# Kernel optimization log

Measured on AMD Instinct MI355X. Metric: run time of the kernel, lower is better.

## Reference

```python
import jax, jax.numpy as jnp
import numpy as np

B, S, D, H = 2, 2048, 2048, 16
HD = D // H
EPS = 1e-5


def layernorm(x, scale, shift):
    mean = jnp.mean(x, axis=-1, keepdims=True)
    var = jnp.mean((x - mean) ** 2, axis=-1, keepdims=True)  # unbiased=False
    return scale * (x - mean) / jnp.sqrt(var + EPS) + shift


def gelu_buggy(x):
    # Faithful to source: tanh is applied ONLY to the constant sqrt(2/pi)
    c = jnp.tanh(jnp.sqrt(jnp.asarray(2.0 / jnp.pi, dtype=x.dtype)))
    return 0.5 * x * (1.0 + c * (x + 0.044715 * x ** 3))


def setup_inputs() -> dict:
    key = jax.random.key(0)
    ks = jax.random.split(key, 10)
    sd = 0.02
    return {
        "x": jax.random.normal(ks[0], (B, S, D), dtype=jnp.float32),
        "wq": jax.random.normal(ks[1], (D, D), dtype=jnp.float32) * sd,
        "wk": jax.random.normal(ks[2], (D, D), dtype=jnp.float32) * sd,
        "wv": jax.random.normal(ks[3], (D, D), dtype=jnp.float32) * sd,
        "wo": jax.random.normal(ks[4], (D, D), dtype=jnp.float32) * sd,
        "bo": jnp.zeros((D,), dtype=jnp.float32),
        "w1": jax.random.normal(ks[5], (D, 4 * D), dtype=jnp.float32) * sd,
        "b1": jnp.zeros((4 * D,), dtype=jnp.float32),
        "w2": jax.random.normal(ks[6], (4 * D, D), dtype=jnp.float32) * sd,
        "b2": jnp.zeros((D,), dtype=jnp.float32),
        "ln_scale": jnp.ones((D,), dtype=jnp.float32),
        "ln_shift": jnp.zeros((D,), dtype=jnp.float32),
    }


def attention(h, wq, wk, wv, wo, bo):
    b, s, _ = h.shape
    q = (h @ wq).reshape(b, s, H, HD).transpose(0, 2, 1, 3)  # [b,h,s,hd]
    k = (h @ wk).reshape(b, s, H, HD).transpose(0, 2, 1, 3)
    v = (h @ wv).reshape(b, s, H, HD).transpose(0, 2, 1, 3)
    scores = jnp.einsum('bhqd,bhkd->bhqk', q, k)
    causal = jnp.tril(jnp.ones((s, s), dtype=bool))
    scores = jnp.where(causal, scores, -jnp.inf)
    w = jax.nn.softmax(scores / jnp.sqrt(jnp.asarray(HD, dtype=h.dtype)), axis=-1)
    ctx = jnp.einsum('bhqk,bhkd->bhqd', w, v).transpose(0, 2, 1, 3).reshape(b, s, D)
    return ctx @ wo + bo


def reference(x, wq, wk, wv, wo, bo, w1, b1, w2, b2, ln_scale, ln_shift):
    # NB: source applies ln1 before BOTH sub-blocks (ln2 unused); dropout is identity (p=0 / eval)
    shortcut = x
    h = layernorm(x, ln_scale, ln_shift)
    h = attention(h, wq, wk, wv, wo, bo)
    x = h + shortcut
    shortcut = x
    h = layernorm(x, ln_scale, ln_shift)
    h = gelu_buggy(h @ w1 + b1) @ w2 + b2
    return h + shortcut
```

## Files before the change

kernel.cpp:

```cpp
#include <hip/hip_runtime.h>
#include <hip/hip_bf16.h>
#include <math.h>


typedef short bf16x8 __attribute__((ext_vector_type(8)));
typedef float f32x4 __attribute__((ext_vector_type(4)));
typedef short short4v __attribute__((ext_vector_type(4)));

#define MFMA16x32(a, b, c) __builtin_amdgcn_mfma_f32_16x16x32_bf16((a), (b), (c), 0, 0, 0)

__device__ __forceinline__ short f2bs(float f) {
    unsigned u = __builtin_bit_cast(unsigned, f);
    unsigned r = (u + 0x7FFFu + ((u >> 16) & 1u)) >> 16;
    return (short)(unsigned short)r;
}

__device__ __forceinline__ void gload_lds16(const void* g, void* l) {
    __builtin_amdgcn_global_load_lds(
        (const __attribute__((address_space(1))) unsigned int*)g,
        (__attribute__((address_space(3))) unsigned int*)l, 16, 0, 0);
}

__global__ __launch_bounds__(256) void transpose_kernel(const float* __restrict__ in,
                                                        short* __restrict__ out,
                                                        int R, int C) {
    __shared__ float tile[32][33];
    const int tx = threadIdx.x & 31;
    const int ty = threadIdx.x >> 5;
    const int c0 = blockIdx.x * 32;
    const int r0 = blockIdx.y * 32;
#pragma unroll
    for (int i = 0; i < 4; ++i) {
        int r = ty + i * 8;
        tile[r][tx] = in[(size_t)(r0 + r) * C + c0 + tx];
    }
    __syncthreads();
#pragma unroll
    for (int i = 0; i < 4; ++i) {
        int r = ty + i * 8;
        out[(size_t)(c0 + r) * R + r0 + tx] = f2bs(tile[tx][r]);
    }
}

__global__ __launch_bounds__(256) void ln_kernel(const float* __restrict__ x,
                                                 const float* __restrict__ sc,
                                                 const float* __restrict__ sh,
                                                 short* __restrict__ out) {
    const int D = 2048;
    const int row = blockIdx.x;
    const int tid = threadIdx.x;
    __shared__ float red[4];
    const float4* xr = (const float4*)(x + (size_t)row * D);
    float4 v0 = xr[tid];
    float4 v1 = xr[tid + 256];
    float vals0[4] = {v0.x, v0.y, v0.z, v0.w};
    float vals1[4] = {v1.x, v1.y, v1.z, v1.w};

    float s = vals0[0] + vals0[1] + vals0[2] + vals0[3] + vals1[0] + vals1[1] + vals1[2] + vals1[3];
#pragma unroll
    for (int off = 32; off; off >>= 1) s += __shfl_xor(s, off);
    if ((tid & 63) == 0) red[tid >> 6] = s;
    __syncthreads();
    float mean = (red[0] + red[1] + red[2] + red[3]) * (1.0f / 2048.0f);
    __syncthreads();

    float q = 0.0f;
#pragma unroll
    for (int j = 0; j < 4; ++j) {
        float t0 = vals0[j] - mean;
        float t1 = vals1[j] - mean;
        q += t0 * t0 + t1 * t1;
    }
#pragma unroll
    for (int off = 32; off; off >>= 1) q += __shfl_xor(q, off);
    if ((tid & 63) == 0) red[tid >> 6] = q;
    __syncthreads();
    float var = (red[0] + red[1] + red[2] + red[3]) * (1.0f / 2048.0f);
    float inv = rsqrtf(var + 1e-5f);

    const int c0 = tid * 4;
    const int c1 = (tid + 256) * 4;
    short4v o0, o1;
#pragma unroll
    for (int j = 0; j < 4; ++j) {
        o0[j] = f2bs(sc[c0 + j] * ((vals0[j] - mean) * inv) + sh[c0 + j]);
        o1[j] = f2bs(sc[c1 + j] * ((vals1[j] - mean) * inv) + sh[c1 + j]);
    }
    *(short4v*)(out + (size_t)row * D + c0) = o0;
    *(short4v*)(out + (size_t)row * D + c1) = o1;
}

template <int EPI>
__global__ __launch_bounds__(512, 1) void gemm_bf16(const short* __restrict__ A,
                                                    const short* __restrict__ Bt,
                                                    int M, int N, int K,
                                                    void* __restrict__ Cout,
                                                    const float* __restrict__ bias,
                                                    const float* __restrict__ res,
                                                    float gconst) {
    extern __shared__ __align__(16) short lds[];
    const int tid = threadIdx.x;
    const int lane = tid & 63;
    const int wid = tid >> 6;
    const int wm = wid >> 1, wn = wid & 1;
    const int l15 = lane & 15, grp = lane >> 4;

    const int gx = gridDim.x;
    int flat = (int)blockIdx.y * gx + (int)blockIdx.x;
    const int cpx = (gx * (int)gridDim.y) >> 3;
    flat = (flat & 7) * cpx + (flat >> 3);
    const int bx = flat % gx, by = flat / gx;
    const long m0 = (long)by * 256, n0 = (long)bx * 128;

    f32x4 zero = {0.f, 0.f, 0.f, 0.f};
    f32x4 acc[4][4];
#pragma unroll
    for (int i = 0; i < 4; i++)
#pragma unroll
        for (int j = 0; j < 4; j++) acc[i][j] = zero;

    auto STAGE = [&](long k0, int b) {
        short* bufA = lds + b * 24576;
        short* bufB = bufA + 16384;
#pragma unroll
        for (int j = 0; j < 4; ++j) {
            int c = tid + j * 512;
            int row = c >> 3, sl = (c & 7) ^ (row & 7);
            gload_lds16(A + (size_t)(m0 + row) * K + k0 + sl * 8,
                        bufA + (size_t)(wid * 64 + j * 512) * 8);
        }
#pragma unroll
        for (int j = 0; j < 2; ++j) {
            int c = tid + j * 512;
            int row = c >> 3, sl = (c & 7) ^ (row & 7);
            gload_lds16(Bt + (size_t)(n0 + row) * K + k0 + sl * 8,
                        bufB + (size_t)(wid * 64 + j * 512) * 8);
        }
    };

    const int nt = K >> 6;
    STAGE(0, 0);
    STAGE(64, 1);
    int cur = 0, nx2 = 2;

    for (int t = 0; t < nt; ++t) {
        if (t + 2 < nt) {
            STAGE((long)(t + 2) * 64, nx2);
            asm volatile("s_waitcnt vmcnt(12)" ::: "memory");
        } else if (t + 1 < nt) {
            asm volatile("s_waitcnt vmcnt(6)" ::: "memory");
        } else {
            asm volatile("s_waitcnt vmcnt(0)" ::: "memory");
        }
        __builtin_amdgcn_s_barrier();
        __builtin_amdgcn_sched_barrier(0);

        const short* bufA = lds + cur * 24576;
        const short* bufB = bufA + 16384;
        bf16x8 af[2][4], bfr[2][4];
#pragma unroll
        for (int kk = 0; kk < 2; ++kk) {
#pragma unroll
            for (int m = 0; m < 4; ++m) {
                int row = wm * 64 + m * 16 + l15;
                af[kk][m] = *(const bf16x8*)(bufA + row * 64 + (((kk * 4 + grp) ^ (row & 7)) * 8));
            }
#pragma unroll
            for (int n = 0; n < 4; ++n) {
                int row = wn * 64 + n * 16 + l15;
                bfr[kk][n] = *(const bf16x8*)(bufB + row * 64 + (((kk * 4 + grp) ^ (row & 7)) * 8));
            }
        }
        __builtin_amdgcn_s_setprio(1);
#pragma unroll
        for (int kk = 0; kk < 2; ++kk)
#pragma unroll
            for (int m = 0; m < 4; ++m)
#pragma unroll
                for (int n = 0; n < 4; ++n)
                    acc[m][n] = MFMA16x32(af[kk][m], bfr[kk][n], acc[m][n]);
        __builtin_amdgcn_s_setprio(0);
        asm volatile("s_waitcnt lgkmcnt(0)" ::: "memory");
        __builtin_amdgcn_s_barrier();
        __builtin_amdgcn_sched_barrier(0);
        cur = (cur == 2) ? 0 : cur + 1;
        nx2 = (nx2 == 2) ? 0 : nx2 + 1;
    }

#pragma unroll
    for (int m = 0; m < 4; m++) {
        long gr = m0 + wm * 64 + m * 16 + grp * 4;
#pragma unroll
        for (int n = 0; n < 4; n++) {
            long gcol = n0 + wn * 64 + n * 16 + l15;
#pragma unroll
            for (int r = 0; r < 4; r++) {
                float vv = acc[m][n][r];
                long idx = (gr + r) * N + gcol;
                if (EPI == 0) {
                    ((short*)Cout)[idx] = f2bs(vv);
                } else if (EPI == 1) {
                    ((float*)Cout)[idx] = vv + bias[gcol] + res[idx];
                } else {
                    float t = vv + bias[gcol];
                    float g = 0.5f * t * (1.0f + gconst * (t + 0.044715f * t * t * t));
                    ((short*)Cout)[idx] = f2bs(g);
                }
            }
        }
    }
}

__global__ __launch_bounds__(256) void reshape_k_kernel(const short* __restrict__ qkv,
                                                        short* __restrict__ Kh) {
    size_t idx = ((size_t)blockIdx.x * 256 + threadIdx.x) * 8;
    int d = (int)(idx & 127);
    int s = (int)((idx >> 7) & 2047);
    int bh = (int)(idx >> 18);
    int b = bh >> 4, h = bh & 15;
    const short* src = qkv + (size_t)(b * 2048 + s) * 6144 + 2048 + h * 128 + d;
    *(bf16x8*)(Kh + idx) = *(const bf16x8*)src;
}

__global__ __launch_bounds__(256) void reshape_v_kernel(const short* __restrict__ qkv,
                                                        short* __restrict__ Vt) {
    __shared__ short tile[32][33];
    const int bid = blockIdx.x;
    const int dt = bid & 3, st = (bid >> 2) & 63, bh = bid >> 8;
    const int b = bh >> 4, h = bh & 15;
    const int s0 = st * 32, d0 = dt * 32;
    const int tx = threadIdx.x & 31, ty = threadIdx.x >> 5;
#pragma unroll
    for (int i = 0; i < 4; ++i) {
        int s = ty + i * 8;
        tile[s][tx] = qkv[(size_t)(b * 2048 + s0 + s) * 6144 + 4096 + h * 128 + d0 + tx];
    }
    __syncthreads();
#pragma unroll
    for (int i = 0; i < 4; ++i) {
        int d = ty + i * 8;
        Vt[((size_t)bh * 128 + d0 + d) * 2048 + s0 + tx] = tile[tx][d];
    }
}

__global__ __launch_bounds__(256) void flash3_kernel(const short* __restrict__ qp,
                                                     const short* __restrict__ Kh,
                                                     const short* __restrict__ Vt,
                                                     short* __restrict__ ctx) {
    const int S = 2048, D = 2048, HD = 128, LD = 6144;
    __shared__ __align__(16) short Ks[2][64 * 128];
    __shared__ __align__(16) short Vs[2][64 * 128];
    __shared__ __align__(16) short Ps[4][16 * 64];
    const int tid = threadIdx.x;
    const int lane = tid & 63, wid = tid >> 6;
    const int l15 = lane & 15, grp = lane >> 4;

    int bid = (int)blockIdx.x;
    bid = (bid & 7) * 64 + (bid >> 3);
    const int p = bid & 15, bh = bid >> 4;
    const int b = bh >> 4, h = bh & 15;
    const int qtH = 31 - p;
    const int nH = qtH + 1;
    const float scale = 0.08838834764831845f;
    const float NEGINF = -__builtin_inff();

    const short* Kbase = Kh + (size_t)bh * S * 128;
    const short* Vbase = Vt + (size_t)bh * 128 * S;
    short* Psw = &Ps[wid][0];

    f32x4 zero = {0.f, 0.f, 0.f, 0.f};
    bf16x8 aq[4];
    float m_[4], l_[4];
    f32x4 o[8];

    int qt = qtH;
    int qw = qt * 64 + wid * 16;
    {
        const short* qrow = qp + (size_t)(b * S + qw + l15) * LD + h * HD;
#pragma unroll
        for (int kc = 0; kc < 4; kc++) aq[kc] = *(const bf16x8*)(qrow + kc * 32 + grp * 8);
    }
#pragma unroll
    for (int r = 0; r < 4; r++) { m_[r] = NEGINF; l_[r] = 0.f; }
#pragma unroll
    for (int n = 0; n < 8; n++) o[n] = zero;

#pragma unroll
    for (int j = 0; j < 4; ++j) {
        int c = tid + j * 256;
        int r = c >> 4, sl = c & 15;
        gload_lds16(Kbase + (size_t)r * 128 + ((sl ^ (r & 7)) * 8),
                    Ks[0] + (size_t)(wid * 64 + j * 256) * 8);
    }
#pragma unroll
    for (int j = 0; j < 4; ++j) {
        int c = tid + j * 256;
        int d = c >> 3, sl = c & 7;
        gload_lds16(Vbase + (size_t)d * S + ((sl ^ (d & 7)) * 8),
                    Vs[0] + (size_t)(wid * 64 + j * 256) * 8);
    }
    __syncthreads();

    int cur = 0;
    for (int i = 0; i < 33; ++i) {
        const int kt = (i < nH) ? i : (i - nH);
        const bool lastT = (kt == qt);

        if (i + 1 < 33) {
            const int ktn = (i + 1 < nH) ? (i + 1) : (i + 1 - nH);
            const long kn0 = (long)ktn * 64;
            const short* Kg = Kbase + kn0 * 128;
            const short* Vg = Vbase + kn0;
            short* kd = Ks[cur ^ 1];
            short* vd = Vs[cur ^ 1];
#pragma unroll
            for (int j = 0; j < 4; ++j) {
                int c = tid + j * 256;
                int r = c >> 4, sl = c & 15;
                gload_lds16(Kg + (size_t)r * 128 + ((sl ^ (r & 7)) * 8),
                            kd + (size_t)(wid * 64 + j * 256) * 8);
            }
#pragma unroll
            for (int j = 0; j < 4; ++j) {
                int c = tid + j * 256;
                int d = c >> 3, sl = c & 7;
                gload_lds16(Vg + (size_t)d * S + ((sl ^ (d & 7)) * 8),
                            vd + (size_t)(wid * 64 + j * 256) * 8);
            }
        }

        const short* Kc = Ks[cur];
        const short* Vc = Vs[cur];

        f32x4 s[4] = {zero, zero, zero, zero};
#pragma unroll
        for (int n = 0; n < 4; ++n) {
            int r = n * 16 + l15;
#pragma unroll
            for (int kc = 0; kc < 4; ++kc) {
                bf16x8 kb = *(const bf16x8*)(Kc + r * 128 + (((kc * 4 + grp) ^ (r & 7)) * 8));
                s[n] = MFMA16x32(aq[kc], kb, s[n]);
            }
        }

        float al[4];
#pragma unroll
        for (int r = 0; r < 4; ++r) {
            float v[4];
#pragma unroll
            for (int n = 0; n < 4; ++n) v[n] = s[n][r] * scale;
            if (lastT) {
                int qrel = wid * 16 + grp * 4 + r;
#pragma unroll
                for (int n = 0; n < 4; ++n)
                    if (n * 16 + l15 > qrel) v[n] = NEGINF;
            }
            float mx = fmaxf(fmaxf(v[0], v[1]), fmaxf(v[2], v[3]));
            mx = fmaxf(mx, __shfl_xor(mx, 1));
            mx = fmaxf(mx, __shfl_xor(mx, 2));
            mx = fmaxf(mx, __shfl_xor(mx, 4));
            mx = fmaxf(mx, __shfl_xor(mx, 8));
            float mn = fmaxf(m_[r], mx);
            float sc_ = __expf(m_[r] - mn);
            float rs = 0.f;
            int q = grp * 4 + r;
#pragma unroll
            for (int n = 0; n < 4; ++n) {
                v[n] = __expf(v[n] - mn);
                rs += v[n];
                Psw[q * 64 + (((n * 2 + (l15 >> 3)) ^ (q & 7)) * 8) + (l15 & 7)] = f2bs(v[n]);
            }
            rs += __shfl_xor(rs, 1);
            rs += __shfl_xor(rs, 2);
            rs += __shfl_xor(rs, 4);
            rs += __shfl_xor(rs, 8);
            l_[r] = l_[r] * sc_ + rs;
            m_[r] = mn;
            al[r] = sc_;
        }
#pragma unroll
        for (int n = 0; n < 8; n++) {
            f32x4 t = o[n];
            t[0] *= al[0]; t[1] *= al[1]; t[2] *= al[2]; t[3] *= al[3];
            o[n] = t;
        }

        bf16x8 pa[2];
#pragma unroll
        for (int kc = 0; kc < 2; ++kc)
            pa[kc] = *(const bf16x8*)(Psw + l15 * 64 + (((kc * 4 + grp) ^ (l15 & 7)) * 8));
#pragma unroll
        for (int n = 0; n < 8; ++n) {
            int d = n * 16 + l15;
#pragma unroll
            for (int kc = 0; kc < 2; ++kc) {
                bf16x8 vb = *(const bf16x8*)(Vc + d * 64 + (((kc * 4 + grp) ^ (d & 7)) * 8));
                o[n] = MFMA16x32(pa[kc], vb, o[n]);
            }
        }

        if (lastT) {
            float inv[4];
#pragma unroll
            for (int r = 0; r < 4; ++r) inv[r] = 1.0f / l_[r];
            short* cb_ = ctx + (size_t)(b * S + qw + grp * 4) * D + h * HD + l15;
#pragma unroll
            for (int n = 0; n < 8; ++n)
#pragma unroll
                for (int r = 0; r < 4; ++r)
                    cb_[(size_t)r * D + n * 16] = f2bs(o[n][r] * inv[r]);
            if (i < 32) {
                qt = 31 - qtH;
                qw = qt * 64 + wid * 16;
                const short* qrow = qp + (size_t)(b * S + qw + l15) * LD + h * HD;
#pragma unroll
                for (int kc = 0; kc < 4; kc++) aq[kc] = *(const bf16x8*)(qrow + kc * 32 + grp * 8);
#pragma unroll
                for (int r = 0; r < 4; r++) { m_[r] = NEGINF; l_[r] = 0.f; }
#pragma unroll
                for (int n = 0; n < 8; n++) o[n] = zero;
            }
        }
        __syncthreads();
        cur ^= 1;
    }
}

extern "C" void kernel_launch(void* const* d_in, const int* in_sizes, int n_in,
                              void* d_out, int out_size, void* d_ws, size_t ws_size,
                              hipStream_t stream) {
    const float* x    = (const float*)d_in[0];
    const float* wq   = (const float*)d_in[1];
    const float* wk   = (const float*)d_in[2];
    const float* wv   = (const float*)d_in[3];
    const float* wo   = (const float*)d_in[4];
    const float* bo   = (const float*)d_in[5];
    const float* w1   = (const float*)d_in[6];
    const float* b1   = (const float*)d_in[7];
    const float* w2   = (const float*)d_in[8];
    const float* b2   = (const float*)d_in[9];
    const float* lnsc = (const float*)d_in[10];
    const float* lnsh = (const float*)d_in[11];

    const int B = 2, S = 2048, D = 2048;
    const int M = B * S;
    const int GEMM_LDS = 3 * 24576 * 2;

    char* p = (char*)d_ws;
    short* wqkvT = (short*)p; p += (size_t)3 * D * D * 2;
    short* woT   = (short*)p; p += (size_t)D * D * 2;
    short* w1T   = (short*)p; p += (size_t)4 * D * D * 2;
    short* w2T   = (short*)p; p += (size_t)4 * D * D * 2;
    short* lnb   = (short*)p; p += (size_t)M * D * 2;
    short* qkvb  = (short*)p;
    short* h1    = qkvb;
    p += (size_t)M * 3 * D * 2;
    short* ctxb  = (short*)p; p += (size_t)M * D * 2;
    float* x2    = (float*)p; p += (size_t)M * D * 4;

    short* Kh = wqkvT;
    short* Vt = (short*)x2;

    const float gconst = tanhf(sqrtf(2.0f / 3.14159265358979323846f));

    hipFuncSetAttribute((const void*)&gemm_bf16<0>, hipFuncAttributeMaxDynamicSharedMemorySize, GEMM_LDS);
    hipFuncSetAttribute((const void*)&gemm_bf16<1>, hipFuncAttributeMaxDynamicSharedMemorySize, GEMM_LDS);
    hipFuncSetAttribute((const void*)&gemm_bf16<2>, hipFuncAttributeMaxDynamicSharedMemorySize, GEMM_LDS);

    dim3 blk(256);
    transpose_kernel<<<dim3(64, 64), blk, 0, stream>>>(wq, wqkvT, D, D);
    transpose_kernel<<<dim3(64, 64), blk, 0, stream>>>(wk, wqkvT + (size_t)D * D, D, D);
    transpose_kernel<<<dim3(64, 64), blk, 0, stream>>>(wv, wqkvT + (size_t)2 * D * D, D, D);
    transpose_kernel<<<dim3(64, 64), blk, 0, stream>>>(wo, woT, D, D);
    transpose_kernel<<<dim3(256, 64), blk, 0, stream>>>(w1, w1T, D, 4 * D);
    transpose_kernel<<<dim3(64, 256), blk, 0, stream>>>(w2, w2T, 4 * D, D);

    ln_kernel<<<dim3(M), blk, 0, stream>>>(x, lnsc, lnsh, lnb);
    gemm_bf16<0><<<dim3(3 * D / 128, M / 256), dim3(512), GEMM_LDS, stream>>>(
        lnb, wqkvT, M, 3 * D, D, qkvb, nullptr, nullptr, 0.f);

    reshape_k_kernel<<<dim3(4096), blk, 0, stream>>>(qkvb, Kh);
    reshape_v_kernel<<<dim3(8192), blk, 0, stream>>>(qkvb, Vt);

    flash3_kernel<<<dim3(512), blk, 0, stream>>>(qkvb, Kh, Vt, ctxb);

    gemm_bf16<1><<<dim3(D / 128, M / 256), dim3(512), GEMM_LDS, stream>>>(
        ctxb, woT, M, D, D, x2, bo, x, 0.f);
    ln_kernel<<<dim3(M), blk, 0, stream>>>(x2, lnsc, lnsh, lnb);
    gemm_bf16<2><<<dim3(4 * D / 128, M / 256), dim3(512), GEMM_LDS, stream>>>(
        lnb, w1T, M, 4 * D, D, h1, b1, nullptr, gconst);
    gemm_bf16<1><<<dim3(D / 128, M / 256), dim3(512), GEMM_LDS, stream>>>(
        h1, w2T, M, D, 4 * D, (float*)d_out, b2, x2, 0.f);
}
```

Before: 655.1 us.

## Add 256x256-tile GEMM with split-K for FFN down-projection

Adds a new GEMM kernel with 256x256 output tiles, double-buffered LDS and raised wave priority around the MFMA block. It is used for the QKV, FFN-up and FFN-down projections, and the down-projection is split two ways along K, with one half written to a partial buffer and summed by a separate add kernel. Larger tiles raise arithmetic intensity and cut operand reloads, while split-K restores enough blocks to fill the GPU. In exchange it costs extra fp32 partial traffic, an extra kernel launch and more register pressure. The partial buffer reuses the transposed-weight region of the workspace.

```diff
diff --git a/kernel.cpp b/kernel.cpp
--- a/kernel.cpp
+++ b/kernel.cpp
@@ -19,6 +19,14 @@
     __builtin_amdgcn_global_load_lds(
         (const __attribute__((address_space(1))) unsigned int*)g,
         (__attribute__((address_space(3))) unsigned int*)l, 16, 0, 0);
+}
+
+template <int N>
+__device__ __forceinline__ void vmw() {
+    if constexpr (N == 0) asm volatile("s_waitcnt vmcnt(0)" ::: "memory");
+    else if constexpr (N == 6) asm volatile("s_waitcnt vmcnt(6)" ::: "memory");
+    else if constexpr (N == 8) asm volatile("s_waitcnt vmcnt(8)" ::: "memory");
+    else if constexpr (N == 12) asm volatile("s_waitcnt vmcnt(12)" ::: "memory");
 }
 
 __global__ __launch_bounds__(256) void transpose_kernel(const float* __restrict__ in,
@@ -90,14 +98,129 @@
     *(short4v*)(out + (size_t)row * D + c1) = o1;
 }
 
+template <int EPI, int SK>
+__global__ __launch_bounds__(512, 2) void gemm256(const short* __restrict__ Aop,
+                                                  const short* __restrict__ Bt,
+                                                  int M, int N, int K,
+                                                  void* __restrict__ Cout,
+                                                  float* __restrict__ part,
+                                                  const float* __restrict__ bias,
+                                                  const float* __restrict__ res,
+                                                  float gconst) {
+    constexpr int TSZ = 256 * 64;
+    extern __shared__ __align__(16) short lds[];
+    const int tid = threadIdx.x;
+    const int lane = tid & 63;
+    const int wid = tid >> 6;
+    const int wm = wid >> 2, wn = wid & 3;
+    const int l15 = lane & 15, grp = lane >> 4;
+
+    const int gx = gridDim.x;
+    int flat = (int)blockIdx.y * gx + (int)blockIdx.x;
+    const int cpx = (gx * (int)gridDim.y) >> 3;
+    flat = (flat & 7) * cpx + (flat >> 3);
+    const int bx = flat % gx;
+    const int byy = flat / gx;
+    const int mtiles = M >> 8;
+    const int myb = byy % mtiles;
+    const int ksl = byy / mtiles;
+    const long m0 = (long)myb * 256, n0 = (long)bx * 256;
+    const int KS = K / SK;
+    const long kbase = (long)ksl * KS;
+    const int nt = KS >> 6;
+
+    f32x4 zero = {0.f, 0.f, 0.f, 0.f};
+    f32x4 acc[8][4];
+#pragma unroll
+    for (int i = 0; i < 8; i++)
+#pragma unroll
+        for (int j = 0; j < 4; j++) acc[i][j] = zero;
+
+    auto STAGE = [&](int t, short* bufA, short* bufB) {
+        const long k0 = kbase + ((long)t << 6);
+#pragma unroll
+        for (int j = 0; j < 4; ++j) {
+            int c = tid + j * 512;
+            int row = c >> 3, sl = (c & 7) ^ (row & 7);
+            gload_lds16(Aop + (size_t)(m0 + row) * K + k0 + sl * 8, bufA + (size_t)c * 8);
+        }
+#pragma unroll
+        for (int j = 0; j < 4; ++j) {
+            int c = tid + j * 512;
+            int row = c >> 3, sl = (c & 7) ^ (row & 7);
+            gload_lds16(Bt + (size_t)(n0 + row) * K + k0 + sl * 8, bufB + (size_t)c * 8);
+        }
+    };
+
+    STAGE(0, lds, lds + 2 * TSZ);
+    STAGE(1, lds + TSZ, lds + 3 * TSZ);
+
+    for (int t = 0; t < nt; ++t) {
+        if (t == nt - 1) { vmw<0>(); } else { vmw<8>(); }
+        __builtin_amdgcn_s_barrier();
+        __builtin_amdgcn_sched_barrier(0);
+        const short* bufA = lds + (t & 1) * TSZ;
+        const short* bufB = lds + 2 * TSZ + (t & 1) * TSZ;
+        __builtin_amdgcn_s_setprio(1);
+#pragma unroll
+        for (int kk = 0; kk < 2; ++kk) {
+            bf16x8 af[8], bfr[4];
+#pragma unroll
+            for (int mi = 0; mi < 8; ++mi) {
+                int row = wm * 128 + mi * 16 + l15;
+                af[mi] = *(const bf16x8*)(bufA + row * 64 + (((kk * 4 + grp) ^ (row & 7)) * 8));
+            }
+#pragma unroll
+            for (int ni = 0; ni < 4; ++ni) {
+                int row = wn * 64 + ni * 16 + l15;
+                bfr[ni] = *(const bf16x8*)(bufB + row * 64 + (((kk * 4 + grp) ^ (row & 7)) * 8));
+            }
+#pragma unroll
+            for (int mi = 0; mi < 8; ++mi)
+#pragma unroll
+                for (int ni = 0; ni < 4; ++ni)
+                    acc[mi][ni] = MFMA16x32(af[mi], bfr[ni], acc[mi][ni]);
+        }
+        __builtin_amdgcn_s_setprio(0);
+        asm volatile("s_waitcnt lgkmcnt(0)" ::: "memory");
+        __builtin_amdgcn_sched_barrier(0);
+        __builtin_amdgcn_s_barrier();
+        if (t + 2 < nt) STAGE(t + 2, lds + (t & 1) * TSZ, lds + 2 * TSZ + (t & 1) * TSZ);
+    }
+
+#pragma unroll
+    for (int mi = 0; mi < 8; mi++) {
+        long gr = m0 + wm * 128 + mi * 16 + grp * 4;
+#pragma unroll
+        for (int ni = 0; ni < 4; ni++) {
+            long gcol = n0 + wn * 64 + ni * 16 + l15;
+#pragma unroll
+            for (int r = 0; r < 4; r++) {
+                float vv = acc[mi][ni][r];
+                long idx = (gr + r) * N + gcol;
+                if constexpr (SK == 2) {
+                    if (ksl == 1) part[idx] = vv;
+                    else ((float*)Cout)[idx] = vv + bias[gcol] + res[idx];
+                } else if constexpr (EPI == 0) {
+                    ((short*)Cout)[idx] = f2bs(vv);
+                } else {
+                    float tv = vv + bias[gcol];
+                    float g = 0.5f * tv * (1.0f + gconst * (tv + 0.044715f * tv * tv * tv));
+                    ((short*)Cout)[idx] = f2bs(g);
+                }
+            }
+        }
+    }
+}
+
 template <int EPI>
-__global__ __launch_bounds__(512, 1) void gemm_bf16(const short* __restrict__ A,
-                                                    const short* __restrict__ Bt,
-                                                    int M, int N, int K,
-                                                    void* __restrict__ Cout,
-                                                    const float* __restrict__ bias,
-                                                    const float* __restrict__ res,
-                                                    float gconst) {
+__global__ __launch_bounds__(512, 1) void gemm3d(const short* __restrict__ A,
+                                                 const short* __restrict__ Bt,
+                                                 int M, int N, int K,
+                                                 void* __restrict__ Cout,
+                                                 const float* __restrict__ bias,
+                                                 const float* __restrict__ res,
+                                                 float gconst) {
     extern __shared__ __align__(16) short lds[];
     const int tid = threadIdx.x;
     const int lane = tid & 63;
@@ -146,11 +269,11 @@
     for (int t = 0; t < nt; ++t) {
         if (t + 2 < nt) {
             STAGE((long)(t + 2) * 64, nx2);
-            asm volatile("s_waitcnt vmcnt(12)" ::: "memory");
+            vmw<12>();
         } else if (t + 1 < nt) {
-            asm volatile("s_waitcnt vmcnt(6)" ::: "memory");
+            vmw<6>();
         } else {
-            asm volatile("s_waitcnt vmcnt(0)" ::: "memory");
+            vmw<0>();
         }
         __builtin_amdgcn_s_barrier();
         __builtin_amdgcn_sched_barrier(0);
@@ -202,12 +325,25 @@
                 } else if (EPI == 1) {
                     ((float*)Cout)[idx] = vv + bias[gcol] + res[idx];
                 } else {
-                    float t = vv + bias[gcol];
-                    float g = 0.5f * t * (1.0f + gconst * (t + 0.044715f * t * t * t));
+                    float t2 = vv + bias[gcol];
+                    float g = 0.5f * t2 * (1.0f + gconst * (t2 + 0.044715f * t2 * t2 * t2));
                     ((short*)Cout)[idx] = f2bs(g);
                 }
             }
         }
+    }
+}
+
+__global__ __launch_bounds__(256) void add_kernel(float* __restrict__ out,
+                                                  const float* __restrict__ part,
+                                                  int n4) {
+    int i = blockIdx.x * 256 + threadIdx.x;
+    int stride = gridDim.x * 256;
+    for (; i < n4; i += stride) {
+        float4 a = ((const float4*)out)[i];
+        float4 b = ((const float4*)part)[i];
+        a.x += b.x; a.y += b.y; a.z += b.z; a.w += b.w;
+        ((float4*)out)[i] = a;
     }
 }
 
@@ -444,7 +580,8 @@
 
     const int B = 2, S = 2048, D = 2048;
     const int M = B * S;
-    const int GEMM_LDS = 3 * 24576 * 2;
+    const int LDS_256 = 4 * 256 * 64 * 2;
+    const int LDS_3D  = 3 * 24576 * 2;
 
     char* p = (char*)d_ws;
     short* wqkvT = (short*)p; p += (size_t)3 * D * D * 2;
@@ -460,12 +597,14 @@
 
     short* Kh = wqkvT;
     short* Vt = (short*)x2;
+    float* part = (float*)d_ws;
 
     const float gconst = tanhf(sqrtf(2.0f / 3.14159265358979323846f));
 
-    hipFuncSetAttribute((const void*)&gemm_bf16<0>, hipFuncAttributeMaxDynamicSharedMemorySize, GEMM_LDS);
-    hipFuncSetAttribute((const void*)&gemm_bf16<1>, hipFuncAttributeMaxDynamicSharedMemorySize, GEMM_LDS);
-    hipFuncSetAttribute((const void*)&gemm_bf16<2>, hipFuncAttributeMaxDynamicSharedMemorySize, GEMM_LDS);
+    hipFuncSetAttribute((const void*)&gemm256<0, 1>, hipFuncAttributeMaxDynamicSharedMemorySize, LDS_256);
+    hipFuncSetAttribute((const void*)&gemm256<2, 1>, hipFuncAttributeMaxDynamicSharedMemorySize, LDS_256);
+    hipFuncSetAttribute((const void*)&gemm256<1, 2>, hipFuncAttributeMaxDynamicSharedMemorySize, LDS_256);
+    hipFuncSetAttribute((const void*)&gemm3d<1>, hipFuncAttributeMaxDynamicSharedMemorySize, LDS_3D);
 
     dim3 blk(256);
     transpose_kernel<<<dim3(64, 64), blk, 0, stream>>>(wq, wqkvT, D, D);
@@ -476,19 +615,20 @@
     transpose_kernel<<<dim3(64, 256), blk, 0, stream>>>(w2, w2T, 4 * D, D);
 
     ln_kernel<<<dim3(M), blk, 0, stream>>>(x, lnsc, lnsh, lnb);
-    gemm_bf16<0><<<dim3(3 * D / 128, M / 256), dim3(512), GEMM_LDS, stream>>>(
-        lnb, wqkvT, M, 3 * D, D, qkvb, nullptr, nullptr, 0.f);
+    gemm256<0, 1><<<dim3(3 * D / 256, M / 256), dim3(512), LDS_256, stream>>>(
+        lnb, wqkvT, M, 3 * D, D, qkvb, nullptr, nullptr, nullptr, 0.f);
 
     reshape_k_kernel<<<dim3(4096), blk, 0, stream>>>(qkvb, Kh);
     reshape_v_kernel<<<dim3(8192), blk, 0, stream>>>(qkvb, Vt);
 
     flash3_kernel<<<dim3(512), blk, 0, stream>>>(qkvb, Kh, Vt, ctxb);
 
-    gemm_bf16<1><<<dim3(D / 128, M / 256), dim3(512), GEMM_LDS, stream>>>(
+    gemm3d<1><<<dim3(D / 128, M / 256), dim3(512), LDS_3D, stream>>>(
         ctxb, woT, M, D, D, x2, bo, x, 0.f);
     ln_kernel<<<dim3(M), blk, 0, stream>>>(x2, lnsc, lnsh, lnb);
-    gemm_bf16<2><<<dim3(4 * D / 128, M / 256), dim3(512), GEMM_LDS, stream>>>(
-        lnb, w1T, M, 4 * D, D, h1, b1, nullptr, gconst);
-    gemm_bf16<1><<<dim3(D / 128, M / 256), dim3(512), GEMM_LDS, stream>>>(
-        h1, w2T, M, D, 4 * D, (float*)d_out, b2, x2, 0.f);
-}
+    gemm256<2, 1><<<dim3(4 * D / 256, M / 256), dim3(512), LDS_256, stream>>>(
+        lnb, w1T, M, 4 * D, D, h1, nullptr, b1, nullptr, gconst);
+    gemm256<1, 2><<<dim3(D / 256, 2 * M / 256), dim3(512), LDS_256, stream>>>(
+        h1, w2T, M, D, 4 * D, (float*)d_out, part, b2, x2, 0.f);
+    add_kernel<<<dim3(2048), blk, 0, stream>>>((float*)d_out, part, M * D / 4);
+}
```

After: 666.4 us. Within noise of the previous version (+1.7%).
